# Performance work log

Hardware: AMD Instinct MI355X
Metric: run time of the kernel (lower is better)

The kernel has to match this reference:

```python
import jax, jax.numpy as jnp
import numpy as np

# search space constants
NUM_INIT_NODES = 2
NUM_NODE_INPUTS = 2
NUM_STEPS = 4
NUM_NODES = NUM_INIT_NODES + NUM_STEPS  # 6
NUM_CELL_GROUPS = 2
NUM_PRIMITIVES = 8
OP_DIM = 48
OP_HID = 48
GCN_DIMS = [128, 128]
BATCH = 32768
N_EDGE = NUM_NODE_INPUTS * NUM_STEPS  # 8


def setup_inputs() -> dict:
    key = jax.random.key(0)
    ks = jax.random.split(key, 8)
    archs = jax.random.randint(ks[0], (BATCH, NUM_CELL_GROUPS, 2, N_EDGE), 0, 6, dtype=jnp.int64 if jax.config.jax_enable_x64 else jnp.int32)
    init_node_emb = jax.random.normal(ks[1], (NUM_INIT_NODES, NUM_NODE_INPUTS * OP_DIM), dtype=jnp.float32)
    op_emb = jax.random.normal(ks[2], (NUM_PRIMITIVES, OP_DIM), dtype=jnp.float32)
    x_hidden_w = jax.random.normal(ks[3], (NUM_NODE_INPUTS * OP_DIM, OP_HID), dtype=jnp.float32) * 0.1
    x_hidden_b = jax.random.normal(ks[4], (OP_HID,), dtype=jnp.float32) * 0.1
    gcn_w1 = jax.random.normal(ks[5], (OP_HID, GCN_DIMS[0]), dtype=jnp.float32) * 0.1
    gcn_w2 = jax.random.normal(ks[6], (GCN_DIMS[0], GCN_DIMS[1]), dtype=jnp.float32) * 0.1
    return {"archs": archs, "init_node_emb": init_node_emb, "op_emb": op_emb,
            "x_hidden_w": x_hidden_w, "x_hidden_b": x_hidden_b,
            "gcn_w1": gcn_w1, "gcn_w2": gcn_w2}


def _get_adj_dense(prev_nodes):
    # prev_nodes: [B2, n_edge] int; scatter-add counts into [B2, N, N]
    b2 = prev_nodes.shape[0]
    t_nodes = jnp.repeat(jnp.arange(NUM_INIT_NODES, NUM_NODES), NUM_NODE_INPUTS)  # [n_edge]
    bidx = jnp.arange(b2)[:, None]
    adj = jnp.zeros((b2, NUM_NODES, NUM_NODES), dtype=jnp.float32)
    adj = adj.at[bidx, t_nodes[None, :], prev_nodes].add(1.0)
    return adj


def reference(archs, init_node_emb, op_emb, x_hidden_w, x_hidden_b, gcn_w1, gcn_w2):
    b, n_cg, _, n_edge = archs.shape
    # dense adjacency per (batch, cell group)
    adjs = _get_adj_dense(archs[:, :, 0, :].reshape(-1, n_edge))
    adjs = adjs.reshape(b, n_cg, NUM_NODES, NUM_NODES)  # [b, g, N, N]
    # op embedding lookup -> intermediate node embeddings
    op_inds = archs[:, :, 1, :]                          # [b, g, n_edge]
    op_embs = op_emb[op_inds]                            # [b, g, n_edge, op_dim]
    inter = op_embs.reshape(b, n_cg, NUM_STEPS, NUM_NODE_INPUTS * OP_DIM)
    init = jnp.broadcast_to(init_node_emb[None, None], (b, n_cg, NUM_INIT_NODES, NUM_NODE_INPUTS * OP_DIM))
    node_embs = jnp.concatenate([init, inter], axis=2)   # [b, g, N, 2*op_dim]
    y = jnp.einsum('bgnd,df->bgnf', node_embs, x_hidden_w) + x_hidden_b  # [b,g,N,op_hid]
    # GCN layers: adj @ (y @ W); relu between layers (not after last); dropout=0 (eval)
    for i, w in enumerate([gcn_w1, gcn_w2]):
        y = jnp.einsum('bgnm,bgmf->bgnf', adjs, jnp.einsum('bgnd,df->bgnf', y, w))
        if i != 1:
            y = jax.nn.relu(y)
    y = jnp.mean(y[:, :, NUM_INIT_NODES:, :], axis=2)    # [b, g, out]
    return y.reshape(b, -1)                               # [b, g*out]
```

## Files before the change

kernel.cpp:

```cpp
#include <hip/hip_runtime.h>
#include <hip/hip_bf16.h>


typedef __attribute__((ext_vector_type(8))) short  bhalf8;
typedef __attribute__((ext_vector_type(4))) float  f32x4;
typedef __attribute__((ext_vector_type(2))) unsigned int u32x2;

#define TAB_ROW 132
#define VROW    136

__device__ __forceinline__ unsigned int bf16rne(float x) {
  unsigned int u = __builtin_bit_cast(unsigned int, x);
  return (u + 0x7FFFu + ((u >> 16) & 1u)) >> 16;
}


__global__ __launch_bounds__(256) void prep_kernel(
    const float* __restrict__ init_emb,
    const float* __restrict__ op_emb,
    const float* __restrict__ wx,
    const float* __restrict__ xb,
    const float* __restrict__ w1,
    const float* __restrict__ w2,
    float* __restrict__ R,
    unsigned short* __restrict__ w2t)
{
  const int tid = threadIdx.x;
  const int b = blockIdx.x;

  if (b < 8) {
    const int fbase = b * 16;
#pragma unroll
    for (int i = 0; i < 8; ++i) {
      int idx = i * 256 + tid;
      int fi = idx >> 7, k = idx & 127;
      int f = fbase + fi;
      w2t[f * 128 + k] = (unsigned short)bf16rne(0.25f * w2[k * 128 + f]);
    }
    return;
  }

  __shared__ float swx[96 * 48];
  __shared__ float sw1[48 * 128];
  __shared__ float smisc[6 * 48 + 2 * 96 + 48];
  __shared__ float sU[14][48];

  for (int i = tid; i < 96 * 48; i += 256) swx[i] = wx[i];
  for (int i = tid; i < 48 * 128; i += 256) sw1[i] = w1[i];
  for (int i = tid; i < 288; i += 256) smisc[i] = op_emb[i];
  if (tid < 192) smisc[288 + tid] = init_emb[tid];
  if (tid < 48)  smisc[480 + tid] = xb[tid];
  __syncthreads();

  const float* sob   = smisc;
  const float* sinit = smisc + 288;
  const float* sxb   = smisc + 480;

  for (int idx = tid; idx < 14 * 48; idx += 256) {
    int row = idx / 48, k = idx - row * 48;
    float s;
    if (row < 6) {
      s = sxb[k];
      for (int j = 0; j < 48; ++j) s += sob[row * 48 + j] * swx[j * 48 + k];
    } else if (row < 12) {
      s = 0.f;
      for (int j = 0; j < 48; ++j) s += sob[(row - 6) * 48 + j] * swx[(48 + j) * 48 + k];
    } else {
      s = sxb[k];
      for (int j = 0; j < 96; ++j) s += sinit[(row - 12) * 96 + j] * swx[j * 48 + k];
    }
    sU[row][k] = s;
  }
  __syncthreads();

  for (int idx = tid; idx < 14 * 128; idx += 256) {
    int row = idx >> 7, f = idx & 127;
    float s = 0.f;
    for (int k = 0; k < 48; ++k) s += sU[row][k] * sw1[k * 128 + f];
    R[idx] = s;
  }
}

__global__ __launch_bounds__(256, 4) void main_kernel(
    const int* __restrict__ archs,
    const float* __restrict__ R,
    const unsigned short* __restrict__ w2t,
    float* __restrict__ out)
{
  __shared__ float          sT[38 * TAB_ROW];
  __shared__ unsigned short sV[64 * VROW];

  const int tid = threadIdx.x;

  for (int idx = tid; idx < 38 * 128; idx += 256) {
    int row = idx >> 7, f = idx & 127;
    float v;
    if (row < 36) {
      int o1 = row / 6, o2 = row - o1 * 6;
      v = R[o1 * 128 + f] + R[(6 + o2) * 128 + f];
    } else {
      v = R[(row - 24) * 128 + f];
    }
    sT[row * TAB_ROW + f] = v;
  }
  __syncthreads();

  const int lane  = tid & 63;
  const int wv    = tid >> 6;
  const int rbase = blockIdx.x * 64 + wv * 16;

  const int rowi = lane >> 2;
  const int sub  = lane & 3;
  const int r    = rbase + rowi;

  const int* ar = archs + r * 16;
  int4 pv0 = *(const int4*)(ar);
  int4 pv1 = *(const int4*)(ar + 4);
  int4 op0 = *(const int4*)(ar + 8);
  int4 op1 = *(const int4*)(ar + 12);

  int soff0 = (op0.x * 6 + op0.y) * TAB_ROW;
  int soff1 = (op0.z * 6 + op0.w) * TAB_ROW;
  int soff2 = (op1.x * 6 + op1.y) * TAB_ROW;
  int soff3 = (op1.z * 6 + op1.w) * TAB_ROW;
  const int s36 = 36 * TAB_ROW, s37 = 37 * TAB_ROW;

  int prev[8] = {pv0.x, pv0.y, pv0.z, pv0.w, pv1.x, pv1.y, pv1.z, pv1.w};
  int aoff[4], boff[4];
  float cf[4];
#pragma unroll
  for (int t = 0; t < 4; ++t) {
    int pa = prev[2 * t], pb = prev[2 * t + 1];
    aoff[t] = (pa == 0) ? s36 : (pa == 1) ? s37 : (pa == 2) ? soff0
            : (pa == 3) ? soff1 : (pa == 4) ? soff2 : soff3;
    boff[t] = (pb == 0) ? s36 : (pb == 1) ? s37 : (pb == 2) ? soff0
            : (pb == 3) ? soff1 : (pb == 4) ? soff2 : soff3;
    int c = 0;
#pragma unroll
    for (int e = 0; e < 8; ++e) c += (prev[e] == t + 2) ? 1 : 0;
    cf[t] = (float)c;
  }

  const int vwbase = (wv * 16 + rowi) * VROW + sub * 4;
#pragma unroll
  for (int it = 0; it < 8; ++it) {
    const int d = sub * 4 + it * 16;
    f32x4 v = {0.f, 0.f, 0.f, 0.f};
#pragma unroll
    for (int t = 0; t < 4; ++t) {
      f32x4 a = *(const f32x4*)&sT[aoff[t] + d];
      f32x4 b = *(const f32x4*)&sT[boff[t] + d];
      f32x4 y = a + b;
      y[0] = fmaxf(y[0], 0.f); y[1] = fmaxf(y[1], 0.f);
      y[2] = fmaxf(y[2], 0.f); y[3] = fmaxf(y[3], 0.f);
      v += cf[t] * y;
    }
    u32x2 p;
    p[0] = bf16rne(v[0]) | (bf16rne(v[1]) << 16);
    p[1] = bf16rne(v[2]) | (bf16rne(v[3]) << 16);
    *(u32x2*)&sV[vwbase + it * 16] = p;
  }

  asm volatile("s_waitcnt lgkmcnt(0)" ::: "memory");

  const int mrow = lane & 15;
  const int kq   = lane >> 4;

  const unsigned short* vb = &sV[(wv * 16 + mrow) * VROW + kq * 8];
  bhalf8 Af[4];
#pragma unroll
  for (int kc = 0; kc < 4; ++kc) Af[kc] = *(const bhalf8*)(vb + kc * 32);

#pragma unroll
  for (int nt = 0; nt < 8; ++nt) {
    f32x4 acc = {0.f, 0.f, 0.f, 0.f};
    const unsigned short* wb = w2t + (nt * 16 + mrow) * 128 + kq * 8;
#pragma unroll
    for (int kc = 0; kc < 4; ++kc) {
      bhalf8 Bf = *(const bhalf8*)(wb + kc * 32);
      acc = __builtin_amdgcn_mfma_f32_16x16x32_bf16(Af[kc], Bf, acc, 0, 0, 0);
    }
#pragma unroll
    for (int j = 0; j < 4; ++j)
      out[(rbase + kq * 4 + j) * 128 + nt * 16 + mrow] = acc[j];
  }
}

extern "C" void kernel_launch(void* const* d_in, const int* in_sizes, int n_in,
                              void* d_out, int out_size, void* d_ws, size_t ws_size,
                              hipStream_t stream) {
  const int*   archs  = (const int*)d_in[0];
  const float* init_e = (const float*)d_in[1];
  const float* op_e   = (const float*)d_in[2];
  const float* wx     = (const float*)d_in[3];
  const float* xb     = (const float*)d_in[4];
  const float* w1     = (const float*)d_in[5];
  const float* w2     = (const float*)d_in[6];

  float*          R   = (float*)d_ws;
  unsigned short* w2t = (unsigned short*)((char*)d_ws + 8192);

  prep_kernel<<<9, 256, 0, stream>>>(init_e, op_e, wx, xb, w1, w2, R, w2t);
  main_kernel<<<1024, 256, 0, stream>>>(archs, R, w2t, (float*)d_out);
}
```

Before: 111.9 us.

## Build MFMA A-fragments directly in registers and spread w2 transpose over more blocks

Each lane now computes the aggregated node features for its own MFMA A-fragment slice straight from the shared table, so the bf16 staging buffer in shared memory and its write/read round trip go away. The archs loads are issued before the table-fill barrier so their global latency overlaps the table build. The w2 transpose in the prep kernel is split over 64 blocks instead of 8. In exchange, lanes in a 16-row group read overlapping table rows, which may raise LDS bank conflicts or register pressure.

New measurement: 109.0 us. 1.03x faster.

```diff
diff --git a/kernel.cpp b/kernel.cpp
--- a/kernel.cpp
+++ b/kernel.cpp
@@ -4,10 +4,8 @@
 
 typedef __attribute__((ext_vector_type(8))) short  bhalf8;
 typedef __attribute__((ext_vector_type(4))) float  f32x4;
-typedef __attribute__((ext_vector_type(2))) unsigned int u32x2;
 
 #define TAB_ROW 132
-#define VROW    136
 
 __device__ __forceinline__ unsigned int bf16rne(float x) {
   unsigned int u = __builtin_bit_cast(unsigned int, x);
@@ -28,15 +26,10 @@
   const int tid = threadIdx.x;
   const int b = blockIdx.x;
 
-  if (b < 8) {
-    const int fbase = b * 16;
-#pragma unroll
-    for (int i = 0; i < 8; ++i) {
-      int idx = i * 256 + tid;
-      int fi = idx >> 7, k = idx & 127;
-      int f = fbase + fi;
-      w2t[f * 128 + k] = (unsigned short)bf16rne(0.25f * w2[k * 128 + f]);
-    }
+  if (b < 64) {
+    int idx = b * 256 + tid;
+    int f = idx >> 7, k = idx & 127;
+    w2t[f * 128 + k] = (unsigned short)bf16rne(0.25f * w2[k * 128 + f]);
     return;
   }
 
@@ -87,10 +80,22 @@
     const unsigned short* __restrict__ w2t,
     float* __restrict__ out)
 {
-  __shared__ float          sT[38 * TAB_ROW];
-  __shared__ unsigned short sV[64 * VROW];
+  __shared__ float sT[38 * TAB_ROW];
 
-  const int tid = threadIdx.x;
+  const int tid  = threadIdx.x;
+  const int lane = tid & 63;
+  const int wv   = tid >> 6;
+  const int rbase = blockIdx.x * 64 + wv * 16;
+
+  const int mrow = lane & 15;
+  const int kq   = lane >> 4;
+  const int r    = rbase + mrow;
+
+  const int* ar = archs + r * 16;
+  int4 pv0 = *(const int4*)(ar);
+  int4 pv1 = *(const int4*)(ar + 4);
+  int4 op0 = *(const int4*)(ar + 8);
+  int4 op1 = *(const int4*)(ar + 12);
 
   for (int idx = tid; idx < 38 * 128; idx += 256) {
     int row = idx >> 7, f = idx & 127;
@@ -104,20 +109,6 @@
     sT[row * TAB_ROW + f] = v;
   }
   __syncthreads();
-
-  const int lane  = tid & 63;
-  const int wv    = tid >> 6;
-  const int rbase = blockIdx.x * 64 + wv * 16;
-
-  const int rowi = lane >> 2;
-  const int sub  = lane & 3;
-  const int r    = rbase + rowi;
-
-  const int* ar = archs + r * 16;
-  int4 pv0 = *(const int4*)(ar);
-  int4 pv1 = *(const int4*)(ar + 4);
-  int4 op0 = *(const int4*)(ar + 8);
-  int4 op1 = *(const int4*)(ar + 12);
 
   int soff0 = (op0.x * 6 + op0.y) * TAB_ROW;
   int soff1 = (op0.z * 6 + op0.w) * TAB_ROW;
@@ -141,35 +132,29 @@
     cf[t] = (float)c;
   }
 
-  const int vwbase = (wv * 16 + rowi) * VROW + sub * 4;
-#pragma unroll
-  for (int it = 0; it < 8; ++it) {
-    const int d = sub * 4 + it * 16;
-    f32x4 v = {0.f, 0.f, 0.f, 0.f};
-#pragma unroll
-    for (int t = 0; t < 4; ++t) {
-      f32x4 a = *(const f32x4*)&sT[aoff[t] + d];
-      f32x4 b = *(const f32x4*)&sT[boff[t] + d];
-      f32x4 y = a + b;
-      y[0] = fmaxf(y[0], 0.f); y[1] = fmaxf(y[1], 0.f);
-      y[2] = fmaxf(y[2], 0.f); y[3] = fmaxf(y[3], 0.f);
-      v += cf[t] * y;
-    }
-    u32x2 p;
-    p[0] = bf16rne(v[0]) | (bf16rne(v[1]) << 16);
-    p[1] = bf16rne(v[2]) | (bf16rne(v[3]) << 16);
-    *(u32x2*)&sV[vwbase + it * 16] = p;
-  }
-
-  asm volatile("s_waitcnt lgkmcnt(0)" ::: "memory");
-
-  const int mrow = lane & 15;
-  const int kq   = lane >> 4;
-
-  const unsigned short* vb = &sV[(wv * 16 + mrow) * VROW + kq * 8];
   bhalf8 Af[4];
 #pragma unroll
-  for (int kc = 0; kc < 4; ++kc) Af[kc] = *(const bhalf8*)(vb + kc * 32);
+  for (int kc = 0; kc < 4; ++kc) {
+    const int d = kq * 8 + kc * 32;
+    unsigned int pk[4];
+#pragma unroll
+    for (int half = 0; half < 2; ++half) {
+      f32x4 v = {0.f, 0.f, 0.f, 0.f};
+      const int dd = d + half * 4;
+#pragma unroll
+      for (int t = 0; t < 4; ++t) {
+        f32x4 a = *(const f32x4*)&sT[aoff[t] + dd];
+        f32x4 b = *(const f32x4*)&sT[boff[t] + dd];
+        f32x4 y = a + b;
+        y[0] = fmaxf(y[0], 0.f); y[1] = fmaxf(y[1], 0.f);
+        y[2] = fmaxf(y[2], 0.f); y[3] = fmaxf(y[3], 0.f);
+        v += cf[t] * y;
+      }
+      pk[2 * half]     = bf16rne(v[0]) | (bf16rne(v[1]) << 16);
+      pk[2 * half + 1] = bf16rne(v[2]) | (bf16rne(v[3]) << 16);
+    }
+    Af[kc] = __builtin_bit_cast(bhalf8, *(__attribute__((ext_vector_type(4))) unsigned int*)pk);
+  }
 
 #pragma unroll
   for (int nt = 0; nt < 8; ++nt) {
@@ -200,6 +185,6 @@
   float*          R   = (float*)d_ws;
   unsigned short* w2t = (unsigned short*)((char*)d_ws + 8192);
 
-  prep_kernel<<<9, 256, 0, stream>>>(init_e, op_e, wx, xb, w1, w2, R, w2t);
+  prep_kernel<<<65, 256, 0, stream>>>(init_e, op_e, wx, xb, w1, w2, R, w2t);
   main_kernel<<<1024, 256, 0, stream>>>(archs, R, w2t, (float*)d_out);
 }
```
